# Performance work log

Measured on AMD Instinct MI355X. Metric: run time of the kernel, lower is better.

## Reference

```python
import jax, jax.numpy as jnp
import numpy as np

N_NODES = 50000
N_EDGES = 800000
IN_DIM = 512
HID = 128
HEADS = 8
HEAD_DIM = HID // HEADS  # 16
N_LAYERS = 3
N_CLASSES = 8


def layer_norm(x, g, b, eps=1e-5):
    mu = jnp.mean(x, axis=-1, keepdims=True)
    var = jnp.mean((x - mu) ** 2, axis=-1, keepdims=True)
    return (x - mu) * jax.lax.rsqrt(var + eps) * g + b


def gat_layer(h, W, a_src, a_dst, bias, src, dst):
    # h: [N, HID]; W: [HID, HEADS*HEAD_DIM]; a_src/a_dst: [HEADS, HEAD_DIM]
    N = h.shape[0]
    hp = (h @ W).reshape(N, HEADS, HEAD_DIM)  # per-head projections
    e_s = jnp.einsum('nhc,hc->nh', hp, a_src)  # [N, H]
    e_d = jnp.einsum('nhc,hc->nh', hp, a_dst)
    logits = jax.nn.leaky_relu(e_s[src] + e_d[dst], negative_slope=0.2)  # [E, H]
    # segment softmax over incoming edges of each dst node
    m = jax.ops.segment_max(logits, dst, num_segments=N)
    p = jnp.exp(logits - m[dst])
    denom = jax.ops.segment_sum(p, dst, num_segments=N)
    alpha = p / (denom[dst] + 1e-16)  # [E, H]
    msg = hp[src] * alpha[:, :, None]  # [E, H, C]
    out = jax.ops.segment_sum(msg, dst, num_segments=N)  # [N, H, C]
    return out.reshape(N, HEADS * HEAD_DIM) + bias


def setup_inputs() -> dict:
    key = jax.random.key(0)
    ks = jax.random.split(key, 32)
    s = 0.05
    inp = {}
    inp['x'] = jax.random.normal(ks[0], (N_NODES, IN_DIM), dtype=jnp.float32)
    inp['edge_src'] = jax.random.randint(ks[1], (N_EDGES,), 0, N_NODES, dtype=jnp.int32)
    inp['edge_dst'] = jax.random.randint(ks[2], (N_EDGES,), 0, N_NODES, dtype=jnp.int32)
    # input projection
    inp['W_in'] = jax.random.normal(ks[3], (IN_DIM, HID)) * s
    inp['b_in'] = jnp.zeros((HID,))
    inp['g_in'] = jnp.ones((HID,))
    inp['be_in'] = jnp.zeros((HID,))
    # stacked GAT layer params
    inp['Wc'] = jax.random.normal(ks[4], (N_LAYERS, HID, HEADS * HEAD_DIM)) * s
    inp['a_src'] = jax.random.normal(ks[5], (N_LAYERS, HEADS, HEAD_DIM)) * s
    inp['a_dst'] = jax.random.normal(ks[6], (N_LAYERS, HEADS, HEAD_DIM)) * s
    inp['bc'] = jnp.zeros((N_LAYERS, HID))
    inp['gc'] = jnp.ones((N_LAYERS, HID))
    inp['bec'] = jnp.zeros((N_LAYERS, HID))
    # classifier
    inp['W1'] = jax.random.normal(ks[7], (HID, HID // 2)) * s
    inp['b1'] = jnp.zeros((HID // 2,))
    inp['g1'] = jnp.ones((HID // 2,))
    inp['be1'] = jnp.zeros((HID // 2,))
    inp['W2'] = jax.random.normal(ks[8], (HID // 2, HID // 4)) * s
    inp['b2'] = jnp.zeros((HID // 4,))
    inp['g2'] = jnp.ones((HID // 4,))
    inp['be2'] = jnp.zeros((HID // 4,))
    inp['W3'] = jax.random.normal(ks[9], (HID // 4, N_CLASSES)) * s
    inp['b3'] = jnp.zeros((N_CLASSES,))
    return inp


def reference(x, W_in, b_in, g_in, be_in, Wc, a_src, a_dst, bc, gc, bec,
              W1, b1, g1, be1, W2, b2, g2, be2, W3, b3, edge_src, edge_dst):
    N = x.shape[0]
    # PyG GATConv adds self-loops by default
    loops = jnp.arange(N, dtype=edge_src.dtype)
    src = jnp.concatenate([edge_src, loops])
    dst = jnp.concatenate([edge_dst, loops])
    # input projection (dropout is identity in eval)
    h = jax.nn.relu(layer_norm(x @ W_in + b_in, g_in, be_in))
    for i in range(N_LAYERS):
        residual = h
        h = gat_layer(h, Wc[i], a_src[i], a_dst[i], bc[i], src, dst)
        h = jax.nn.relu(layer_norm(h, gc[i], bec[i]))
        if i > 0:
            h = h + residual
    # classifier head
    h = jax.nn.relu(layer_norm(h @ W1 + b1, g1, be1))
    h = jax.nn.relu(layer_norm(h @ W2 + b2, g2, be2))
    return h @ W3 + b3
```

## Files before the change

kernel.cpp:

```cpp
#include <hip/hip_runtime.h>
#include <math.h>

#define N_NODES 50000
#define N_EDGES 800000
#define IN_DIM 512
#define HID 128
#define HEADS 8
#define HEAD_DIM 16
#define N_LAYERS 3
#define N_CLASSES 8
#define LOG2E 1.4426950408889634f

typedef __attribute__((ext_vector_type(8))) short short8;
typedef __attribute__((ext_vector_type(4))) short short4v;
typedef __attribute__((ext_vector_type(4))) float f32x4;

__device__ inline unsigned short f2bf(float f) {
  unsigned u = __float_as_uint(f);
  u = (u + 0x7fffu + ((u >> 16) & 1u)) >> 16;
  return (unsigned short)u;
}
__device__ inline float bflo(unsigned u) { return __uint_as_float(u << 16); }
__device__ inline float bfhi(unsigned u) { return __uint_as_float(u & 0xffff0000u); }

__global__ __launch_bounds__(256) void k_cvt_w(
    const float* __restrict__ W_in, const float* __restrict__ Wc,
    const float* __restrict__ W1, const float* __restrict__ W2,
    const float* __restrict__ W3,
    unsigned short* __restrict__ Wt_in, unsigned short* __restrict__ Wt_c,
    unsigned short* __restrict__ W1t, unsigned short* __restrict__ W2t,
    unsigned short* __restrict__ W3t) {
  int i = blockIdx.x * blockDim.x + threadIdx.x;
  if (i < IN_DIM * HID) {
    int c = i >> 9, k = i & 511;
    Wt_in[i] = f2bf(W_in[k * HID + c]);
  }
  if (i < N_LAYERS * HID * HID) {
    int l = i >> 14, r = i & 16383, c = r >> 7, k = r & 127;
    Wt_c[i] = f2bf(Wc[l * HID * HID + k * HID + c]);
  }
  if (i < 64 * 128) {
    int c = i >> 7, k = i & 127;
    W1t[i] = f2bf(W1[k * 64 + c]);
  }
  if (i < 32 * 64) {
    int c = i >> 6, k = i & 63;
    W2t[i] = f2bf(W2[k * 32 + c]);
  }
  if (i < 16 * 32) {
    int c = i >> 5, k = i & 31;
    W3t[i] = (c < 8) ? f2bf(W3[k * N_CLASSES + c]) : 0;
  }
}

template <int K>
__device__ inline void gemm_mainloop(const float* __restrict__ A, size_t row0,
                                     const unsigned short* __restrict__ Wt,
                                     unsigned short* lds_a, unsigned short* lds_b,
                                     f32x4 acc[8]) {
  const int tid = threadIdx.x;
  const int lane = tid & 63, wid = tid >> 6;
#pragma unroll
  for (int f = 0; f < 8; ++f)
#pragma unroll
    for (int j = 0; j < 4; ++j) acc[f][j] = 0.f;

  for (int kb = 0; kb < K; kb += 64) {
#pragma unroll
    for (int j = 0; j < 4; ++j) {
      int i = tid + j * 256;
      int r = i >> 4, kq = (i & 15) * 4;
      size_t rg = row0 + r;
      if (rg >= N_NODES) rg = N_NODES - 1;
      float4 v = *(const float4*)(A + rg * K + kb + kq);
      short4v b4;
      b4[0] = (short)f2bf(v.x); b4[1] = (short)f2bf(v.y);
      b4[2] = (short)f2bf(v.z); b4[3] = (short)f2bf(v.w);
      int idx = (r * 64 + kq) ^ ((r & 7) << 3);
      *(short4v*)&lds_a[idx] = b4;
    }
#pragma unroll
    for (int j = 0; j < 4; ++j) {
      int i = tid + j * 256;
      int c = i >> 3, kq = (i & 7) * 8;
      short8 w = *(const short8*)(Wt + (size_t)c * K + kb + kq);
      int idx = (c * 64 + kq) ^ ((c & 7) << 3);
      *(short8*)&lds_b[idx] = w;
    }
    __syncthreads();

    int arow = wid * 16 + (lane & 15);
    int kq8 = (lane >> 4) * 8;
    short8 a0 = *(short8*)&lds_a[(arow * 64 + kq8) ^ ((arow & 7) << 3)];
    short8 a1 = *(short8*)&lds_a[(arow * 64 + 32 + kq8) ^ ((arow & 7) << 3)];
#pragma unroll
    for (int f = 0; f < 8; ++f) {
      int c = f * 16 + (lane & 15);
      short8 b0 = *(short8*)&lds_b[(c * 64 + kq8) ^ ((c & 7) << 3)];
      short8 b1 = *(short8*)&lds_b[(c * 64 + 32 + kq8) ^ ((c & 7) << 3)];
      acc[f] = __builtin_amdgcn_mfma_f32_16x16x32_bf16(a0, b0, acc[f], 0, 0, 0);
      acc[f] = __builtin_amdgcn_mfma_f32_16x16x32_bf16(a1, b1, acc[f], 0, 0, 0);
    }
    __syncthreads();
  }
}

__global__ __launch_bounds__(256) void k_gemm_in(
    const float* __restrict__ x, const unsigned short* __restrict__ Wt,
    const float* __restrict__ b, const float* __restrict__ g,
    const float* __restrict__ be, float* __restrict__ h0) {
  __shared__ unsigned short lds_a[64 * 64];
  __shared__ unsigned short lds_b[128 * 64];
  f32x4 acc[8];
  size_t row0 = (size_t)blockIdx.x * 64;
  gemm_mainloop<IN_DIM>(x, row0, Wt, lds_a, lds_b, acc);

  int lane = threadIdx.x & 63, wid = threadIdx.x >> 6;
  int cbase = lane & 15;
  float s[4] = {0.f, 0.f, 0.f, 0.f}, q[4] = {0.f, 0.f, 0.f, 0.f};
  float gg[8], bb[8];
#pragma unroll
  for (int f = 0; f < 8; ++f) {
    int c = f * 16 + cbase;
    float bias = b[c];
    gg[f] = g[c]; bb[f] = be[c];
#pragma unroll
    for (int j = 0; j < 4; ++j) {
      float v = acc[f][j] + bias;
      acc[f][j] = v;
      s[j] += v; q[j] += v * v;
    }
  }
#pragma unroll
  for (int off = 8; off >= 1; off >>= 1)
#pragma unroll
    for (int j = 0; j < 4; ++j) {
      s[j] += __shfl_xor(s[j], off);
      q[j] += __shfl_xor(q[j], off);
    }
#pragma unroll
  for (int j = 0; j < 4; ++j) {
    size_t row = row0 + wid * 16 + (lane >> 4) * 4 + j;
    if (row < N_NODES) {
      float mu = s[j] * (1.f / 128.f);
      float var = q[j] * (1.f / 128.f) - mu * mu;
      float rs = rsqrtf(var + 1e-5f);
#pragma unroll
      for (int f = 0; f < 8; ++f) {
        float y = (acc[f][j] - mu) * rs * gg[f] + bb[f];
        h0[row * HID + f * 16 + cbase] = fmaxf(y, 0.f);
      }
    }
  }
}

__global__ __launch_bounds__(256) void k_gemm_gat(
    const float* __restrict__ h, const unsigned short* __restrict__ Wt,
    const float* __restrict__ asrc, const float* __restrict__ adst,
    unsigned short* __restrict__ hp_bf, float* __restrict__ es,
    float* __restrict__ ed) {
  __shared__ unsigned short lds_a[64 * 64];
  __shared__ unsigned short lds_b[128 * 64];
  f32x4 acc[8];
  size_t row0 = (size_t)blockIdx.x * 64;
  gemm_mainloop<HID>(h, row0, Wt, lds_a, lds_b, acc);

  int lane = threadIdx.x & 63, wid = threadIdx.x >> 6;
  int cbase = lane & 15;
#pragma unroll
  for (int f = 0; f < 8; ++f) {
    float av = asrc[f * 16 + cbase], bv = adst[f * 16 + cbase];
    float eS[4], eD[4];
#pragma unroll
    for (int j = 0; j < 4; ++j) { eS[j] = acc[f][j] * av; eD[j] = acc[f][j] * bv; }
#pragma unroll
    for (int off = 8; off >= 1; off >>= 1)
#pragma unroll
      for (int j = 0; j < 4; ++j) {
        eS[j] += __shfl_xor(eS[j], off);
        eD[j] += __shfl_xor(eD[j], off);
      }
#pragma unroll
    for (int j = 0; j < 4; ++j) {
      size_t row = row0 + wid * 16 + (lane >> 4) * 4 + j;
      if (row < N_NODES) {
        hp_bf[row * HID + f * 16 + cbase] = f2bf(acc[f][j]);
        if (cbase == 0) {
          es[row * HEADS + f] = eS[j] * LOG2E;
          ed[row * HEADS + f] = eD[j] * LOG2E;
        }
      }
    }
  }
}

__global__ void k_zero_int(int* __restrict__ p, int nn) {
  int i = blockIdx.x * blockDim.x + threadIdx.x;
  if (i < nn) p[i] = 0;
}

__global__ void k_count(const int* __restrict__ dst, int* __restrict__ deg) {
  int e = blockIdx.x * blockDim.x + threadIdx.x;
  if (e < N_EDGES) atomicAdd(&deg[dst[e]], 1);
}

__global__ __launch_bounds__(1024) void k_scan(const int* __restrict__ deg,
                                               int* __restrict__ offs) {
  __shared__ int wsum[16];
  __shared__ int s_carry;
  int tid = threadIdx.x, lane = tid & 63, wid = tid >> 6;
  if (tid == 0) { s_carry = 0; offs[0] = 0; }
  __syncthreads();
  for (int base = 0; base < N_NODES; base += 8192) {
    int i0 = base + tid * 8;
    int v[8];
    int run = 0;
#pragma unroll
    for (int k = 0; k < 8; ++k) {
      int d = (i0 + k < N_NODES) ? deg[i0 + k] : 0;
      run += d; v[k] = run;
    }
    int ws = run;
#pragma unroll
    for (int off = 1; off < 64; off <<= 1) {
      int t = __shfl_up(ws, off);
      if (lane >= off) ws += t;
    }
    if (lane == 63) wsum[wid] = ws;
    __syncthreads();
    int carry = s_carry;
    int prefix = carry;
    for (int w = 0; w < wid; ++w) prefix += wsum[w];
    int excl = prefix + ws - run;
#pragma unroll
    for (int k = 0; k < 8; ++k)
      if (i0 + k < N_NODES) offs[i0 + k + 1] = excl + v[k];
    __syncthreads();
    if (tid == 0) {
      int tot = 0;
      for (int w = 0; w < 16; ++w) tot += wsum[w];
      s_carry = carry + tot;
    }
    __syncthreads();
  }
}

__global__ void k_scatter(const int* __restrict__ src, const int* __restrict__ dst,
                          const int* __restrict__ offs, int* __restrict__ cur,
                          int* __restrict__ col) {
  int e = blockIdx.x * blockDim.x + threadIdx.x;
  if (e < N_EDGES) {
    int d = dst[e];
    int pos = offs[d] + atomicAdd(&cur[d], 1);
    col[pos] = src[e];
  }
}

__global__ __launch_bounds__(256) void k_gat_agg(
    const unsigned short* __restrict__ hp_bf, const float* __restrict__ es,
    const float* __restrict__ ed, const int* __restrict__ offs,
    const int* __restrict__ col, const float* __restrict__ bc,
    const float* __restrict__ gc, const float* __restrict__ bec,
    const float* __restrict__ h_res, float* __restrict__ h_out, int use_res) {
  int lane = threadIdx.x & 63;
  int n = blockIdx.x * 4 + (threadIdx.x >> 6);
  if (n >= N_NODES) return;
  int head = lane >> 3;
  int sub = lane & 7;
  int hbase = head * 8;
  const unsigned* hpu = (const unsigned*)hp_bf;

  float edv = ed[(size_t)n * HEADS + head];
  float z0 = es[(size_t)n * HEADS + head] + edv;
  z0 = fmaxf(z0, 0.2f * z0);
  float p0 = exp2f(z0);
  unsigned su = hpu[(size_t)n * 64 + lane];

  float den0 = p0, ax0 = p0 * bflo(su), ay0 = p0 * bfhi(su);
  float den1 = 0.f, ax1 = 0.f, ay1 = 0.f;

  int s0 = offs[n], s1 = offs[n + 1];
  int base = s0;
  for (; base + 8 <= s1; base += 8) {
    int se = col[base + sub];
    float z = es[(size_t)se * HEADS + head] + edv;
    z = fmaxf(z, 0.2f * z);
    float p = exp2f(z);
#pragma unroll
    for (int k = 0; k < 8; k += 2) {
      float pk0 = __shfl(p, hbase + k);
      float pk1 = __shfl(p, hbase + k + 1);
      int sk0 = __shfl(se, k);
      int sk1 = __shfl(se, k + 1);
      unsigned h0 = hpu[(size_t)sk0 * 64 + lane];
      unsigned h1 = hpu[(size_t)sk1 * 64 + lane];
      den0 += pk0;
      ax0 = fmaf(pk0, bflo(h0), ax0);
      ay0 = fmaf(pk0, bfhi(h0), ay0);
      den1 += pk1;
      ax1 = fmaf(pk1, bflo(h1), ax1);
      ay1 = fmaf(pk1, bfhi(h1), ay1);
    }
  }
  int rem = s1 - base;
  if (rem > 0) {
    int e = base + (sub < rem ? sub : rem - 1);
    int se = col[e];
    float z = es[(size_t)se * HEADS + head] + edv;
    z = fmaxf(z, 0.2f * z);
    float p = (sub < rem) ? exp2f(z) : 0.f;
    for (int k = 0; k < rem; ++k) {
      float pk = __shfl(p, hbase + k);
      int sk = __shfl(se, k);
      unsigned hk = hpu[(size_t)sk * 64 + lane];
      den0 += pk;
      ax0 = fmaf(pk, bflo(hk), ax0);
      ay0 = fmaf(pk, bfhi(hk), ay0);
    }
  }
  float den = den0 + den1 + 1e-16f;
  float rden = 1.f / den;
  float v0 = (ax0 + ax1) * rden + bc[2 * lane];
  float v1 = (ay0 + ay1) * rden + bc[2 * lane + 1];

  float s = v0 + v1, q = v0 * v0 + v1 * v1;
#pragma unroll
  for (int off = 32; off >= 1; off >>= 1) {
    s += __shfl_xor(s, off);
    q += __shfl_xor(q, off);
  }
  float mu = s * (1.f / 128.f);
  float var = q * (1.f / 128.f) - mu * mu;
  float rs = rsqrtf(var + 1e-5f);
  float y0 = fmaxf((v0 - mu) * rs * gc[2 * lane] + bec[2 * lane], 0.f);
  float y1 = fmaxf((v1 - mu) * rs * gc[2 * lane + 1] + bec[2 * lane + 1], 0.f);
  if (use_res) {
    float2 r = ((const float2*)h_res)[(size_t)n * 64 + lane];
    y0 += r.x; y1 += r.y;
  }
  ((float2*)h_out)[(size_t)n * 64 + lane] = make_float2(y0, y1);
}

__global__ __launch_bounds__(256) void k_head_mfma(
    const float* __restrict__ h,
    const unsigned short* __restrict__ W1t, const float* __restrict__ b1,
    const float* __restrict__ g1, const float* __restrict__ be1,
    const unsigned short* __restrict__ W2t, const float* __restrict__ b2,
    const float* __restrict__ g2, const float* __restrict__ be2,
    const unsigned short* __restrict__ W3t, const float* __restrict__ b3,
    float* __restrict__ out) {
  __shared__ unsigned short lds_a[64 * 128];
  __shared__ unsigned short lds_b1[64 * 128];
  __shared__ unsigned short lds_h1[64 * 64];
  __shared__ unsigned short lds_b2[32 * 64];
  __shared__ unsigned short lds_h2[64 * 32];
  __shared__ unsigned short lds_b3[16 * 32];
  int tid = threadIdx.x, lane = tid & 63, wid = tid >> 6;
  size_t row0 = (size_t)blockIdx.x * 64;

#pragma unroll
  for (int jj = 0; jj < 8; ++jj) {
    int i = tid + jj * 256;
    int r = i >> 5, kq = (i & 31) * 4;
    size_t rg = row0 + r;
    if (rg >= N_NODES) rg = N_NODES - 1;
    float4 v = *(const float4*)(h + rg * HID + kq);
    short4v b4;
    b4[0] = (short)f2bf(v.x); b4[1] = (short)f2bf(v.y);
    b4[2] = (short)f2bf(v.z); b4[3] = (short)f2bf(v.w);
    int idx = (r * 128 + kq) ^ ((r & 7) << 3);
    *(short4v*)&lds_a[idx] = b4;
  }
#pragma unroll
  for (int jj = 0; jj < 4; ++jj) {
    int i = tid + jj * 256;
    int c = i >> 4, kq = (i & 15) * 8;
    short8 w = *(const short8*)(W1t + c * 128 + kq);
    int idx = (c * 128 + kq) ^ ((c & 7) << 3);
    *(short8*)&lds_b1[idx] = w;
  }
  {
    int c = tid >> 3, kq = (tid & 7) * 8;
    if (c < 32) {
      short8 w = *(const short8*)(W2t + c * 64 + kq);
      int idx = (c * 64 + kq) ^ ((c & 7) << 3);
      *(short8*)&lds_b2[idx] = w;
    }
  }
  if (tid < 64) {
    int c = tid >> 2, kq = (tid & 3) * 8;
    short8 w = *(const short8*)(W3t + c * 32 + kq);
    int idx = (c * 32 + kq) ^ ((c & 3) << 3);
    *(short8*)&lds_b3[idx] = w;
  }
  __syncthreads();

  int arow = wid * 16 + (lane & 15);
  int kq8 = (lane >> 4) * 8;
  int cbase = lane & 15;

  f32x4 acc1[4];
#pragma unroll
  for (int f = 0; f < 4; ++f)
#pragma unroll
    for (int j = 0; j < 4; ++j) acc1[f][j] = 0.f;
  {
    short8 a0 = *(short8*)&lds_a[(arow * 128 + kq8) ^ ((arow & 7) << 3)];
    short8 a1 = *(short8*)&lds_a[(arow * 128 + 32 + kq8) ^ ((arow & 7) << 3)];
    short8 a2 = *(short8*)&lds_a[(arow * 128 + 64 + kq8) ^ ((arow & 7) << 3)];
    short8 a3 = *(short8*)&lds_a[(arow * 128 + 96 + kq8) ^ ((arow & 7) << 3)];
#pragma unroll
    for (int f = 0; f < 4; ++f) {
      int c = f * 16 + cbase;
      short8 b0 = *(short8*)&lds_b1[(c * 128 + kq8) ^ ((c & 7) << 3)];
      short8 bb1 = *(short8*)&lds_b1[(c * 128 + 32 + kq8) ^ ((c & 7) << 3)];
      short8 b2v = *(short8*)&lds_b1[(c * 128 + 64 + kq8) ^ ((c & 7) << 3)];
      short8 b3v = *(short8*)&lds_b1[(c * 128 + 96 + kq8) ^ ((c & 7) << 3)];
      acc1[f] = __builtin_amdgcn_mfma_f32_16x16x32_bf16(a0, b0, acc1[f], 0, 0, 0);
      acc1[f] = __builtin_amdgcn_mfma_f32_16x16x32_bf16(a1, bb1, acc1[f], 0, 0, 0);
      acc1[f] = __builtin_amdgcn_mfma_f32_16x16x32_bf16(a2, b2v, acc1[f], 0, 0, 0);
      acc1[f] = __builtin_amdgcn_mfma_f32_16x16x32_bf16(a3, b3v, acc1[f], 0, 0, 0);
    }
  }
  {
    float s[4] = {0, 0, 0, 0}, q[4] = {0, 0, 0, 0};
#pragma unroll
    for (int f = 0; f < 4; ++f) {
      int c = f * 16 + cbase;
      float bias = b1[c];
#pragma unroll
      for (int j = 0; j < 4; ++j) {
        float v = acc1[f][j] + bias;
        acc1[f][j] = v;
        s[j] += v; q[j] += v * v;
      }
    }
#pragma unroll
    for (int off = 8; off >= 1; off >>= 1)
#pragma unroll
      for (int j = 0; j < 4; ++j) {
        s[j] += __shfl_xor(s[j], off);
        q[j] += __shfl_xor(q[j], off);
      }
#pragma unroll
    for (int j = 0; j < 4; ++j) {
      int row = wid * 16 + (lane >> 4) * 4 + j;
      float mu = s[j] * (1.f / 64.f);
      float var = q[j] * (1.f / 64.f) - mu * mu;
      float rs = rsqrtf(var + 1e-5f);
#pragma unroll
      for (int f = 0; f < 4; ++f) {
        int c = f * 16 + cbase;
        float y = fmaxf((acc1[f][j] - mu) * rs * g1[c] + be1[c], 0.f);
        lds_h1[(row * 64 + c) ^ ((row & 7) << 3)] = f2bf(y);
      }
    }
  }
  __syncthreads();

  f32x4 acc2[2];
#pragma unroll
  for (int f = 0; f < 2; ++f)
#pragma unroll
    for (int j = 0; j < 4; ++j) acc2[f][j] = 0.f;
  {
    short8 a0 = *(short8*)&lds_h1[(arow * 64 + kq8) ^ ((arow & 7) << 3)];
    short8 a1 = *(short8*)&lds_h1[(arow * 64 + 32 + kq8) ^ ((arow & 7) << 3)];
#pragma unroll
    for (int f = 0; f < 2; ++f) {
      int c = f * 16 + cbase;
      short8 b0 = *(short8*)&lds_b2[(c * 64 + kq8) ^ ((c & 7) << 3)];
      short8 bb1 = *(short8*)&lds_b2[(c * 64 + 32 + kq8) ^ ((c & 7) << 3)];
      acc2[f] = __builtin_amdgcn_mfma_f32_16x16x32_bf16(a0, b0, acc2[f], 0, 0, 0);
      acc2[f] = __builtin_amdgcn_mfma_f32_16x16x32_bf16(a1, bb1, acc2[f], 0, 0, 0);
    }
  }
  {
    float s[4] = {0, 0, 0, 0}, q[4] = {0, 0, 0, 0};
#pragma unroll
    for (int f = 0; f < 2; ++f) {
      int c = f * 16 + cbase;
      float bias = b2[c];
#pragma unroll
      for (int j = 0; j < 4; ++j) {
        float v = acc2[f][j] + bias;
        acc2[f][j] = v;
        s[j] += v; q[j] += v * v;
      }
    }
#pragma unroll
    for (int off = 8; off >= 1; off >>= 1)
#pragma unroll
      for (int j = 0; j < 4; ++j) {
        s[j] += __shfl_xor(s[j], off);
        q[j] += __shfl_xor(q[j], off);
      }
#pragma unroll
    for (int j = 0; j < 4; ++j) {
      int row = wid * 16 + (lane >> 4) * 4 + j;
      float mu = s[j] * (1.f / 32.f);
      float var = q[j] * (1.f / 32.f) - mu * mu;
      float rs = rsqrtf(var + 1e-5f);
#pragma unroll
      for (int f = 0; f < 2; ++f) {
        int c = f * 16 + cbase;
        float y = fmaxf((acc2[f][j] - mu) * rs * g2[c] + be2[c], 0.f);
        lds_h2[(row * 32 + c) ^ ((row & 3) << 3)] = f2bf(y);
      }
    }
  }
  __syncthreads();

  f32x4 acc3;
#pragma unroll
  for (int j = 0; j < 4; ++j) acc3[j] = 0.f;
  {
    short8 a = *(short8*)&lds_h2[(arow * 32 + kq8) ^ ((arow & 3) << 3)];
    short8 b = *(short8*)&lds_b3[(cbase * 32 + kq8) ^ ((cbase & 3) << 3)];
    acc3 = __builtin_amdgcn_mfma_f32_16x16x32_bf16(a, b, acc3, 0, 0, 0);
  }
  if (cbase < N_CLASSES) {
    float bias = b3[cbase];
#pragma unroll
    for (int j = 0; j < 4; ++j) {
      size_t row = row0 + wid * 16 + (lane >> 4) * 4 + j;
      if (row < N_NODES) out[row * N_CLASSES + cbase] = acc3[j] + bias;
    }
  }
}

extern "C" void kernel_launch(void* const* d_in, const int* in_sizes, int n_in,
                              void* d_out, int out_size, void* d_ws, size_t ws_size,
                              hipStream_t stream) {
  const float* x     = (const float*)d_in[0];
  const int*   esrc  = (const int*)d_in[1];
  const int*   edst  = (const int*)d_in[2];
  const float* W_in  = (const float*)d_in[3];
  const float* b_in  = (const float*)d_in[4];
  const float* g_in  = (const float*)d_in[5];
  const float* be_in = (const float*)d_in[6];
  const float* Wc    = (const float*)d_in[7];
  const float* a_src = (const float*)d_in[8];
  const float* a_dst = (const float*)d_in[9];
  const float* bc    = (const float*)d_in[10];
  const float* gc    = (const float*)d_in[11];
  const float* bec   = (const float*)d_in[12];
  const float* W1    = (const float*)d_in[13];
  const float* b1    = (const float*)d_in[14];
  const float* g1    = (const float*)d_in[15];
  const float* be1   = (const float*)d_in[16];
  const float* W2    = (const float*)d_in[17];
  const float* b2    = (const float*)d_in[18];
  const float* g2    = (const float*)d_in[19];
  const float* be2   = (const float*)d_in[20];
  const float* W3    = (const float*)d_in[21];
  const float* b3    = (const float*)d_in[22];

  float* ws = (float*)d_ws;
  const size_t NH = (size_t)N_NODES * HID;
  float* hA = ws;
  float* hB = hA + NH;
  float* es = hB + NH;
  float* ed = es + (size_t)N_NODES * HEADS;
  unsigned short* hp_bf = (unsigned short*)(ed + (size_t)N_NODES * HEADS);
  int* deg  = (int*)(hp_bf + NH);
  int* cur  = deg + N_NODES;
  int* offs = cur + N_NODES;
  int* col  = offs + N_NODES + 1;
  uintptr_t wp = (uintptr_t)(col + N_EDGES);
  wp = (wp + 15) & ~(uintptr_t)15;
  unsigned short* Wt_in = (unsigned short*)wp;
  unsigned short* Wt_c  = Wt_in + (size_t)IN_DIM * HID;
  unsigned short* W1t   = Wt_c + (size_t)N_LAYERS * HID * HID;
  unsigned short* W2t   = W1t + 64 * 128;
  unsigned short* W3t   = W2t + 32 * 64;

  k_cvt_w<<<256, 256, 0, stream>>>(W_in, Wc, W1, W2, W3, Wt_in, Wt_c, W1t, W2t, W3t);

  k_gemm_in<<<(N_NODES + 63) / 64, 256, 0, stream>>>(x, Wt_in, b_in, g_in, be_in, hA);

  k_zero_int<<<(2 * N_NODES + 255) / 256, 256, 0, stream>>>(deg, 2 * N_NODES);
  k_count<<<(N_EDGES + 255) / 256, 256, 0, stream>>>(edst, deg);
  k_scan<<<1, 1024, 0, stream>>>(deg, offs);
  k_scatter<<<(N_EDGES + 255) / 256, 256, 0, stream>>>(esrc, edst, offs, cur, col);

  float* hcur = hA;
  float* hnext = hB;
  for (int l = 0; l < N_LAYERS; ++l) {
    k_gemm_gat<<<(N_NODES + 63) / 64, 256, 0, stream>>>(
        hcur, Wt_c + (size_t)l * HID * HID,
        a_src + (size_t)l * HEADS * HEAD_DIM, a_dst + (size_t)l * HEADS * HEAD_DIM,
        hp_bf, es, ed);
    k_gat_agg<<<(N_NODES + 3) / 4, 256, 0, stream>>>(
        hp_bf, es, ed, offs, col,
        bc + (size_t)l * HID, gc + (size_t)l * HID, bec + (size_t)l * HID,
        hcur, hnext, l > 0 ? 1 : 0);
    float* t = hcur; hcur = hnext; hnext = t;
  }

  k_head_mfma<<<(N_NODES + 63) / 64, 256, 0, stream>>>(
      hcur, W1t, b1, g1, be1, W2t, b2, g2, be2, W3t, b3, (float*)d_out);
}
```

Baseline: 350.2 us.

## Split GAT aggregation into head-pair passes over blocked bf16 layout

Projected features are written in a head-pair-blocked layout, so each aggregation pass gathers a compact 64-byte slice per source node, which should improve cache hit rates on the random gathers. The aggregation kernel now runs four passes (two heads each) with four edge groups per wave instead of shuffle-broadcast loops. Each pass writes normalized messages to a new fp32 temporary, and a separate kernel applies bias, layernorm, relu and residual. The degree-buffer zeroing is folded into the weight-prep kernel. The cost is an extra global round trip through the temporary, one extra launch per layer, and re-reading col, es and offs in every pass.

```diff
diff --git a/kernel.cpp b/kernel.cpp
--- a/kernel.cpp
+++ b/kernel.cpp
@@ -23,14 +23,15 @@
 __device__ inline float bflo(unsigned u) { return __uint_as_float(u << 16); }
 __device__ inline float bfhi(unsigned u) { return __uint_as_float(u & 0xffff0000u); }
 
-__global__ __launch_bounds__(256) void k_cvt_w(
+__global__ __launch_bounds__(256) void k_prep(
     const float* __restrict__ W_in, const float* __restrict__ Wc,
     const float* __restrict__ W1, const float* __restrict__ W2,
     const float* __restrict__ W3,
     unsigned short* __restrict__ Wt_in, unsigned short* __restrict__ Wt_c,
     unsigned short* __restrict__ W1t, unsigned short* __restrict__ W2t,
-    unsigned short* __restrict__ W3t) {
+    unsigned short* __restrict__ W3t, int* __restrict__ degcur) {
   int i = blockIdx.x * blockDim.x + threadIdx.x;
+  if (i < 2 * N_NODES) degcur[i] = 0;
   if (i < IN_DIM * HID) {
     int c = i >> 9, k = i & 511;
     Wt_in[i] = f2bf(W_in[k * HID + c]);
@@ -157,7 +158,7 @@
 __global__ __launch_bounds__(256) void k_gemm_gat(
     const float* __restrict__ h, const unsigned short* __restrict__ Wt,
     const float* __restrict__ asrc, const float* __restrict__ adst,
-    unsigned short* __restrict__ hp_bf, float* __restrict__ es,
+    unsigned short* __restrict__ hp_blk, float* __restrict__ es,
     float* __restrict__ ed) {
   __shared__ unsigned short lds_a[64 * 64];
   __shared__ unsigned short lds_b[128 * 64];
@@ -184,7 +185,8 @@
     for (int j = 0; j < 4; ++j) {
       size_t row = row0 + wid * 16 + (lane >> 4) * 4 + j;
       if (row < N_NODES) {
-        hp_bf[row * HID + f * 16 + cbase] = f2bf(acc[f][j]);
+        hp_blk[((size_t)(f >> 1) * N_NODES + row) * 32 + (f & 1) * 16 + cbase] =
+            f2bf(acc[f][j]);
         if (cbase == 0) {
           es[row * HEADS + f] = eS[j] * LOG2E;
           ed[row * HEADS + f] = eD[j] * LOG2E;
@@ -192,11 +194,6 @@
       }
     }
   }
-}
-
-__global__ void k_zero_int(int* __restrict__ p, int nn) {
-  int i = blockIdx.x * blockDim.x + threadIdx.x;
-  if (i < nn) p[i] = 0;
 }
 
 __global__ void k_count(const int* __restrict__ dst, int* __restrict__ deg) {
@@ -257,71 +254,64 @@
 }
 
 __global__ __launch_bounds__(256) void k_gat_agg(
-    const unsigned short* __restrict__ hp_bf, const float* __restrict__ es,
+    const unsigned short* __restrict__ hp_blk, const float* __restrict__ es,
     const float* __restrict__ ed, const int* __restrict__ offs,
-    const int* __restrict__ col, const float* __restrict__ bc,
+    const int* __restrict__ col, float* __restrict__ vtmp) {
+  const int NB4 = (N_NODES + 3) / 4;
+  int bid = blockIdx.x;
+  int pass = bid / NB4, nb = bid - pass * NB4;
+  int lane = threadIdx.x & 63, wid = threadIdx.x >> 6;
+  int n = nb * 4 + wid;
+  if (n >= N_NODES) return;
+  int grp = lane >> 4, li = lane & 15;
+  int gh = 2 * pass + (li >> 3);
+  const unsigned* hpu = (const unsigned*)hp_blk + (size_t)pass * N_NODES * 16;
+
+  float edv = ed[(size_t)n * HEADS + gh];
+  float den = 0.f, ax = 0.f, ay = 0.f;
+  if (grp == 0) {
+    float z0 = es[(size_t)n * HEADS + gh] + edv;
+    z0 = fmaxf(z0, 0.2f * z0);
+    float p0 = exp2f(z0);
+    unsigned su = hpu[(size_t)n * 16 + li];
+    den = p0; ax = p0 * bflo(su); ay = p0 * bfhi(su);
+  }
+  int s1 = offs[n + 1];
+#pragma unroll 2
+  for (int e = offs[n] + grp; e < s1; e += 4) {
+    int se = col[e];
+    float z = es[(size_t)se * HEADS + gh] + edv;
+    z = fmaxf(z, 0.2f * z);
+    float p = exp2f(z);
+    unsigned hu = hpu[(size_t)se * 16 + li];
+    den += p;
+    ax = fmaf(p, bflo(hu), ax);
+    ay = fmaf(p, bfhi(hu), ay);
+  }
+#pragma unroll
+  for (int off = 16; off <= 32; off <<= 1) {
+    den += __shfl_xor(den, off);
+    ax  += __shfl_xor(ax, off);
+    ay  += __shfl_xor(ay, off);
+  }
+  if (grp == 0) {
+    float rden = 1.f / (den + 1e-16f);
+    ((float2*)vtmp)[((size_t)pass * N_NODES + n) * 16 + li] =
+        make_float2(ax * rden, ay * rden);
+  }
+}
+
+__global__ __launch_bounds__(256) void k_ln_res(
+    const float* __restrict__ vtmp, const float* __restrict__ bc,
     const float* __restrict__ gc, const float* __restrict__ bec,
     const float* __restrict__ h_res, float* __restrict__ h_out, int use_res) {
   int lane = threadIdx.x & 63;
   int n = blockIdx.x * 4 + (threadIdx.x >> 6);
   if (n >= N_NODES) return;
-  int head = lane >> 3;
-  int sub = lane & 7;
-  int hbase = head * 8;
-  const unsigned* hpu = (const unsigned*)hp_bf;
-
-  float edv = ed[(size_t)n * HEADS + head];
-  float z0 = es[(size_t)n * HEADS + head] + edv;
-  z0 = fmaxf(z0, 0.2f * z0);
-  float p0 = exp2f(z0);
-  unsigned su = hpu[(size_t)n * 64 + lane];
-
-  float den0 = p0, ax0 = p0 * bflo(su), ay0 = p0 * bfhi(su);
-  float den1 = 0.f, ax1 = 0.f, ay1 = 0.f;
-
-  int s0 = offs[n], s1 = offs[n + 1];
-  int base = s0;
-  for (; base + 8 <= s1; base += 8) {
-    int se = col[base + sub];
-    float z = es[(size_t)se * HEADS + head] + edv;
-    z = fmaxf(z, 0.2f * z);
-    float p = exp2f(z);
-#pragma unroll
-    for (int k = 0; k < 8; k += 2) {
-      float pk0 = __shfl(p, hbase + k);
-      float pk1 = __shfl(p, hbase + k + 1);
-      int sk0 = __shfl(se, k);
-      int sk1 = __shfl(se, k + 1);
-      unsigned h0 = hpu[(size_t)sk0 * 64 + lane];
-      unsigned h1 = hpu[(size_t)sk1 * 64 + lane];
-      den0 += pk0;
-      ax0 = fmaf(pk0, bflo(h0), ax0);
-      ay0 = fmaf(pk0, bfhi(h0), ay0);
-      den1 += pk1;
-      ax1 = fmaf(pk1, bflo(h1), ax1);
-      ay1 = fmaf(pk1, bfhi(h1), ay1);
-    }
-  }
-  int rem = s1 - base;
-  if (rem > 0) {
-    int e = base + (sub < rem ? sub : rem - 1);
-    int se = col[e];
-    float z = es[(size_t)se * HEADS + head] + edv;
-    z = fmaxf(z, 0.2f * z);
-    float p = (sub < rem) ? exp2f(z) : 0.f;
-    for (int k = 0; k < rem; ++k) {
-      float pk = __shfl(p, hbase + k);
-      int sk = __shfl(se, k);
-      unsigned hk = hpu[(size_t)sk * 64 + lane];
-      den0 += pk;
-      ax0 = fmaf(pk, bflo(hk), ax0);
-      ay0 = fmaf(pk, bfhi(hk), ay0);
-    }
-  }
-  float den = den0 + den1 + 1e-16f;
-  float rden = 1.f / den;
-  float v0 = (ax0 + ax1) * rden + bc[2 * lane];
-  float v1 = (ay0 + ay1) * rden + bc[2 * lane + 1];
+  int blk = lane >> 4, li = lane & 15;
+  float2 v = ((const float2*)vtmp)[((size_t)blk * N_NODES + n) * 16 + li];
+  int c0 = 2 * lane;
+  float v0 = v.x + bc[c0], v1 = v.y + bc[c0 + 1];
 
   float s = v0 + v1, q = v0 * v0 + v1 * v1;
 #pragma unroll
@@ -332,8 +322,8 @@
   float mu = s * (1.f / 128.f);
   float var = q * (1.f / 128.f) - mu * mu;
   float rs = rsqrtf(var + 1e-5f);
-  float y0 = fmaxf((v0 - mu) * rs * gc[2 * lane] + bec[2 * lane], 0.f);
-  float y1 = fmaxf((v1 - mu) * rs * gc[2 * lane + 1] + bec[2 * lane + 1], 0.f);
+  float y0 = fmaxf((v0 - mu) * rs * gc[c0] + bec[c0], 0.f);
+  float y1 = fmaxf((v1 - mu) * rs * gc[c0 + 1] + bec[c0 + 1], 0.f);
   if (use_res) {
     float2 r = ((const float2*)h_res)[(size_t)n * 64 + lane];
     y0 += r.x; y1 += r.y;
@@ -560,10 +550,11 @@
   const size_t NH = (size_t)N_NODES * HID;
   float* hA = ws;
   float* hB = hA + NH;
-  float* es = hB + NH;
+  float* vtmp = hB + NH;
+  float* es = vtmp + NH;
   float* ed = es + (size_t)N_NODES * HEADS;
-  unsigned short* hp_bf = (unsigned short*)(ed + (size_t)N_NODES * HEADS);
-  int* deg  = (int*)(hp_bf + NH);
+  unsigned short* hp_blk = (unsigned short*)(ed + (size_t)N_NODES * HEADS);
+  int* deg  = (int*)(hp_blk + NH);
   int* cur  = deg + N_NODES;
   int* offs = cur + N_NODES;
   int* col  = offs + N_NODES + 1;
@@ -575,25 +566,26 @@
   unsigned short* W2t   = W1t + 64 * 128;
   unsigned short* W3t   = W2t + 32 * 64;
 
-  k_cvt_w<<<256, 256, 0, stream>>>(W_in, Wc, W1, W2, W3, Wt_in, Wt_c, W1t, W2t, W3t);
+  k_prep<<<(2 * N_NODES + 255) / 256, 256, 0, stream>>>(
+      W_in, Wc, W1, W2, W3, Wt_in, Wt_c, W1t, W2t, W3t, deg);
 
   k_gemm_in<<<(N_NODES + 63) / 64, 256, 0, stream>>>(x, Wt_in, b_in, g_in, be_in, hA);
 
-  k_zero_int<<<(2 * N_NODES + 255) / 256, 256, 0, stream>>>(deg, 2 * N_NODES);
   k_count<<<(N_EDGES + 255) / 256, 256, 0, stream>>>(edst, deg);
   k_scan<<<1, 1024, 0, stream>>>(deg, offs);
   k_scatter<<<(N_EDGES + 255) / 256, 256, 0, stream>>>(esrc, edst, offs, cur, col);
 
+  const int NB4 = (N_NODES + 3) / 4;
   float* hcur = hA;
   float* hnext = hB;
   for (int l = 0; l < N_LAYERS; ++l) {
     k_gemm_gat<<<(N_NODES + 63) / 64, 256, 0, stream>>>(
         hcur, Wt_c + (size_t)l * HID * HID,
         a_src + (size_t)l * HEADS * HEAD_DIM, a_dst + (size_t)l * HEADS * HEAD_DIM,
-        hp_bf, es, ed);
-    k_gat_agg<<<(N_NODES + 3) / 4, 256, 0, stream>>>(
-        hp_bf, es, ed, offs, col,
-        bc + (size_t)l * HID, gc + (size_t)l * HID, bec + (size_t)l * HID,
+        hp_blk, es, ed);
+    k_gat_agg<<<4 * NB4, 256, 0, stream>>>(hp_blk, es, ed, offs, col, vtmp);
+    k_ln_res<<<NB4, 256, 0, stream>>>(
+        vtmp, bc + (size_t)l * HID, gc + (size_t)l * HID, bec + (size_t)l * HID,
         hcur, hnext, l > 0 ? 1 : 0);
     float* t = hcur; hcur = hnext; hnext = t;
   }
```

Result: slower. 518.5 us (+48.1%).
